# Performance work log

Hardware: AMD Instinct MI355X
Metric: run time of the kernel (lower is better)

Reference implementation:

```python
import jax, jax.numpy as jnp
import numpy as np

EPS = 1e-8  # torch CosineSimilarity default eps


def setup_inputs() -> dict:
    key = jax.random.key(0)
    k_emb, k_idx, k_w1, k_w2 = jax.random.split(key, 4)
    N, H, E = 50000, 128, 800000
    emb = jax.random.normal(k_emb, (N, H), dtype=jnp.float32)
    edge_index = jax.random.randint(k_idx, (2, E), 0, N, dtype=jnp.int64)
    # xavier_uniform for square H x H: limit = sqrt(6 / (H + H))
    lim = float(np.sqrt(6.0 / (H + H)))
    W1 = jax.random.uniform(k_w1, (H, H), dtype=jnp.float32, minval=-lim, maxval=lim)
    W2 = jax.random.uniform(k_w2, (H, H), dtype=jnp.float32, minval=-lim, maxval=lim)
    b1 = jnp.zeros((H,), dtype=jnp.float32)
    b2 = jnp.zeros((H,), dtype=jnp.float32)
    return {"emb": emb, "edge_index": edge_index, "W1": W1, "b1": b1, "W2": W2, "b2": b2}


def reference(emb, edge_index, W1, b1, W2, b2):
    col, row = edge_index[0], edge_index[1]

    def mlp(x):  # Linear -> (Dropout: identity at eval) -> ELU -> Linear
        h = jax.nn.elu(x @ W1.T + b1)
        return h @ W2.T + b2

    f1 = mlp(emb[col])  # [E, H]
    f2 = mlp(emb[row])  # [E, H]
    n1 = jnp.maximum(jnp.sqrt(jnp.sum(f1 * f1, axis=1)), EPS)
    n2 = jnp.maximum(jnp.sqrt(jnp.sum(f2 * f2, axis=1)), EPS)
    return jnp.sum(f1 * f2, axis=1) / (n1 * n2)  # [E]
```

## Files before the change

### kernel.cpp

```cpp
#include <hip/hip_runtime.h>
#include <math.h>

#define H 128
#define MROWS 64
#define XS 136

#if defined(__has_builtin)
# if __has_builtin(__builtin_amdgcn_sdot4)
#  define HAVE_SDOT4 1
# endif
#endif

typedef __attribute__((ext_vector_type(8))) short short8;
typedef __attribute__((ext_vector_type(4))) float floatx4;

__device__ __forceinline__ unsigned short f2bf(float f) {
    unsigned u = __float_as_uint(f);
    return (unsigned short)((u + 0x7FFFu + ((u >> 16) & 1u)) >> 16);
}

__global__ __launch_bounds__(256, 3) void mlp_mfma(
    const float* __restrict__ emb, const float* __restrict__ W1,
    const float* __restrict__ W2, const float* __restrict__ b1,
    const float* __restrict__ b2,
    signed char* __restrict__ qtab, float* __restrict__ scl, int N)
{
    __shared__ unsigned short Wl[H * XS];
    __shared__ unsigned short hs[MROWS * XS];

    const int tid   = threadIdx.x;
    const int wave  = tid >> 6, lane = tid & 63;
    const int quad  = lane >> 4, l15 = lane & 15;
    const int node0 = blockIdx.x * MROWS;

    const int  mrow = wave * 16 + l15;
    const int  grow = node0 + mrow;
    const bool rv   = grow < N;

    #pragma unroll
    for (int i = 0; i < 16; ++i) {
        int f = i * 1024 + tid * 4;
        int row = f >> 7, c = f & 127;
        float4 v = *(const float4*)(W1 + f);
        ushort4 b;
        b.x = f2bf(v.x); b.y = f2bf(v.y); b.z = f2bf(v.z); b.w = f2bf(v.w);
        *(ushort4*)(Wl + row * XS + c) = b;
    }

    short8 afr[4];
    #pragma unroll
    for (int ks = 0; ks < 4; ++ks) {
        float4 u0 = make_float4(0.f, 0.f, 0.f, 0.f);
        float4 u1 = make_float4(0.f, 0.f, 0.f, 0.f);
        if (rv) {
            const float* p = emb + (size_t)grow * H + ks * 32 + quad * 8;
            u0 = *(const float4*)p;
            u1 = *(const float4*)(p + 4);
        }
        short8 a;
        a[0] = (short)f2bf(u0.x); a[1] = (short)f2bf(u0.y);
        a[2] = (short)f2bf(u0.z); a[3] = (short)f2bf(u0.w);
        a[4] = (short)f2bf(u1.x); a[5] = (short)f2bf(u1.y);
        a[6] = (short)f2bf(u1.z); a[7] = (short)f2bf(u1.w);
        afr[ks] = a;
    }
    __syncthreads();

    #pragma unroll
    for (int nt = 0; nt < 8; ++nt) {
        floatx4 acc = {0.f, 0.f, 0.f, 0.f};
        #pragma unroll
        for (int ks = 0; ks < 4; ++ks) {
            short8 bfr = *(const short8*)(Wl + (nt * 16 + l15) * XS + ks * 32 + quad * 8);
            acc = __builtin_amdgcn_mfma_f32_16x16x32_bf16(afr[ks], bfr, acc, 0, 0, 0);
        }
        const int col = nt * 16 + l15;
        const float bb1 = b1[col];
        #pragma unroll
        for (int r = 0; r < 4; ++r) {
            float v = acc[r] + bb1;
            v = v > 0.f ? v : (__expf(v) - 1.f);
            hs[(wave * 16 + quad * 4 + r) * XS + col] = f2bf(v);
        }
    }
    __syncthreads();

    #pragma unroll
    for (int ks = 0; ks < 4; ++ks)
        afr[ks] = *(const short8*)(hs + mrow * XS + ks * 32 + quad * 8);
    #pragma unroll
    for (int i = 0; i < 16; ++i) {
        int f = i * 1024 + tid * 4;
        int row = f >> 7, c = f & 127;
        float4 v = *(const float4*)(W2 + f);
        ushort4 b;
        b.x = f2bf(v.x); b.y = f2bf(v.y); b.z = f2bf(v.z); b.w = f2bf(v.w);
        *(ushort4*)(Wl + row * XS + c) = b;
    }
    __syncthreads();

    floatx4 av[8];
    float sq[4] = {0.f, 0.f, 0.f, 0.f};
    float am[4] = {0.f, 0.f, 0.f, 0.f};
    #pragma unroll
    for (int nt = 0; nt < 8; ++nt) {
        floatx4 acc = {0.f, 0.f, 0.f, 0.f};
        #pragma unroll
        for (int ks = 0; ks < 4; ++ks) {
            short8 bfr = *(const short8*)(Wl + (nt * 16 + l15) * XS + ks * 32 + quad * 8);
            acc = __builtin_amdgcn_mfma_f32_16x16x32_bf16(afr[ks], bfr, acc, 0, 0, 0);
        }
        const float bb2 = b2[nt * 16 + l15];
        #pragma unroll
        for (int r = 0; r < 4; ++r) {
            float v = acc[r] + bb2;
            av[nt][r] = v;
            sq[r] += v * v;
            am[r] = fmaxf(am[r], fabsf(v));
        }
    }
    #pragma unroll
    for (int r = 0; r < 4; ++r) {
        float s = sq[r], a = am[r];
        #pragma unroll
        for (int m = 8; m; m >>= 1) {
            s += __shfl_xor(s, m);
            a = fmaxf(a, __shfl_xor(a, m));
        }
        sq[r] = s; am[r] = a;
    }
    #pragma unroll
    for (int r = 0; r < 4; ++r) {
        const int row = wave * 16 + quad * 4 + r;
        const int G = node0 + row;
        if (G < N) {
            const float a = fmaxf(am[r], 1e-20f);
            if (l15 == 0) {
                float nn = sqrtf(sq[r]);
                if (nn < 1e-8f) nn = 1e-8f;
                scl[G] = a / (nn * 127.f);
            }
            const float qs = 127.f / a;
            unsigned pk0 = 0, pk1 = 0;
            #pragma unroll
            for (int nt = 0; nt < 4; ++nt) {
                int q = (int)rintf(av[nt][r] * qs);
                q = q > 127 ? 127 : (q < -127 ? -127 : q);
                pk0 |= ((unsigned)(q & 255)) << (8 * nt);
            }
            #pragma unroll
            for (int nt = 4; nt < 8; ++nt) {
                int q = (int)rintf(av[nt][r] * qs);
                q = q > 127 ? 127 : (q < -127 ? -127 : q);
                pk1 |= ((unsigned)(q & 255)) << (8 * (nt - 4));
            }
            *(uint2*)(qtab + (size_t)G * H + l15 * 8) = make_uint2(pk0, pk1);
        }
    }
}

__device__ __forceinline__ int dot4s(unsigned a, unsigned b) {
    int s = 0;
    #pragma unroll
    for (int j = 0; j < 4; ++j)
        s += (int)((signed char)(a >> (8 * j))) * (int)((signed char)(b >> (8 * j)));
    return s;
}

__device__ __forceinline__ int dot16(uint4 a, uint4 b) {
#if defined(HAVE_SDOT4)
    int s = __builtin_amdgcn_sdot4((int)a.x, (int)b.x, 0, false);
    s = __builtin_amdgcn_sdot4((int)a.y, (int)b.y, s, false);
    s = __builtin_amdgcn_sdot4((int)a.z, (int)b.z, s, false);
    s = __builtin_amdgcn_sdot4((int)a.w, (int)b.w, s, false);
    return s;
#else
    return dot4s(a.x, b.x) + dot4s(a.y, b.y) + dot4s(a.z, b.z) + dot4s(a.w, b.w);
#endif
}

__global__ __launch_bounds__(256) void edge_cos(
    const int* __restrict__ ei, const signed char* __restrict__ qtab,
    const float* __restrict__ scl, float* __restrict__ out, int E)
{
    const int tid = threadIdx.x;
    const int sub = tid & 7;
    const int g   = (blockIdx.x * 256 + tid) >> 3;
    const int e0  = g * 4;
    if (e0 >= E) return;

    int cc[4], rr[4];
    #pragma unroll
    for (int k = 0; k < 4; ++k) {
        int e = e0 + k;
        if (e >= E) e = E - 1;
        cc[k] = __builtin_nontemporal_load(ei + e);
        rr[k] = __builtin_nontemporal_load(ei + e + E);
    }
    uint4 ua[4], ub[4];
    #pragma unroll
    for (int k = 0; k < 4; ++k) {
        ua[k] = *(const uint4*)(qtab + (size_t)cc[k] * H + sub * 16);
        ub[k] = *(const uint4*)(qtab + (size_t)rr[k] * H + sub * 16);
    }
    float sc[4];
    #pragma unroll
    for (int k = 0; k < 4; ++k) sc[k] = scl[cc[k]] * scl[rr[k]];

    #pragma unroll
    for (int k = 0; k < 4; ++k) {
        int s = dot16(ua[k], ub[k]);
        s += __shfl_xor(s, 4);
        s += __shfl_xor(s, 2);
        s += __shfl_xor(s, 1);
        if (sub == 0 && e0 + k < E)
            __builtin_nontemporal_store((float)s * sc[k], out + e0 + k);
    }
}

extern "C" void kernel_launch(void* const* d_in, const int* in_sizes, int n_in,
                              void* d_out, int out_size, void* d_ws, size_t ws_size,
                              hipStream_t stream) {
    const float* emb = (const float*)d_in[0];
    const int*   ei  = (const int*)d_in[1];
    const float* W1  = (const float*)d_in[2];
    const float* b1  = (const float*)d_in[3];
    const float* W2  = (const float*)d_in[4];
    const float* b2  = (const float*)d_in[5];
    float*       out = (float*)d_out;

    const int N = in_sizes[0] / H;
    const int E = in_sizes[1] / 2;

    signed char* qtab = (signed char*)d_ws;
    float*       sclp = (float*)(qtab + (size_t)N * H);

    mlp_mfma<<<(N + MROWS - 1) / MROWS, 256, 0, stream>>>(emb, W1, W2, b1, b2,
                                                          qtab, sclp, N);
    edge_cos<<<(E + 127) / 128, 256, 0, stream>>>(ei, qtab, sclp, out, E);
}
```

Before: 119.8 us.

## Pre-convert weights to bf16 once and use single-wave MLP blocks reading weights from global

```diff
diff --git a/kernel.cpp b/kernel.cpp
--- a/kernel.cpp
+++ b/kernel.cpp
@@ -2,7 +2,6 @@
 #include <math.h>
 
 #define H 128
-#define MROWS 64
 #define XS 136
 
 #if defined(__has_builtin)
@@ -13,39 +12,33 @@
 
 typedef __attribute__((ext_vector_type(8))) short short8;
 typedef __attribute__((ext_vector_type(4))) float floatx4;
+typedef __attribute__((ext_vector_type(4))) int intx4;
 
 __device__ __forceinline__ unsigned short f2bf(float f) {
     unsigned u = __float_as_uint(f);
     return (unsigned short)((u + 0x7FFFu + ((u >> 16) & 1u)) >> 16);
 }
 
-__global__ __launch_bounds__(256, 3) void mlp_mfma(
-    const float* __restrict__ emb, const float* __restrict__ W1,
-    const float* __restrict__ W2, const float* __restrict__ b1,
-    const float* __restrict__ b2,
+__global__ void prep_weights(const float* __restrict__ W1,
+                             const float* __restrict__ W2,
+                             unsigned short* __restrict__ Wbf) {
+    int i = blockIdx.x * 256 + threadIdx.x;
+    if (i < 16384)       Wbf[i] = f2bf(W1[i]);
+    else if (i < 32768)  Wbf[i] = f2bf(W2[i - 16384]);
+}
+
+__global__ __launch_bounds__(64, 4) void mlp_wave(
+    const float* __restrict__ emb, const unsigned short* __restrict__ Wbf,
+    const float* __restrict__ b1, const float* __restrict__ b2,
     signed char* __restrict__ qtab, float* __restrict__ scl, int N)
 {
-    __shared__ unsigned short Wl[H * XS];
-    __shared__ unsigned short hs[MROWS * XS];
-
-    const int tid   = threadIdx.x;
-    const int wave  = tid >> 6, lane = tid & 63;
+    __shared__ unsigned short hs[16 * XS];
+
+    const int lane  = threadIdx.x;
     const int quad  = lane >> 4, l15 = lane & 15;
-    const int node0 = blockIdx.x * MROWS;
-
-    const int  mrow = wave * 16 + l15;
-    const int  grow = node0 + mrow;
+    const int node0 = blockIdx.x * 16;
+    const int grow  = node0 + l15;
     const bool rv   = grow < N;
-
-    #pragma unroll
-    for (int i = 0; i < 16; ++i) {
-        int f = i * 1024 + tid * 4;
-        int row = f >> 7, c = f & 127;
-        float4 v = *(const float4*)(W1 + f);
-        ushort4 b;
-        b.x = f2bf(v.x); b.y = f2bf(v.y); b.z = f2bf(v.z); b.w = f2bf(v.w);
-        *(ushort4*)(Wl + row * XS + c) = b;
-    }
 
     short8 afr[4];
     #pragma unroll
@@ -64,14 +57,13 @@
         a[6] = (short)f2bf(u1.z); a[7] = (short)f2bf(u1.w);
         afr[ks] = a;
     }
-    __syncthreads();
 
     #pragma unroll
     for (int nt = 0; nt < 8; ++nt) {
         floatx4 acc = {0.f, 0.f, 0.f, 0.f};
         #pragma unroll
         for (int ks = 0; ks < 4; ++ks) {
-            short8 bfr = *(const short8*)(Wl + (nt * 16 + l15) * XS + ks * 32 + quad * 8);
+            short8 bfr = *(const short8*)(Wbf + (nt * 16 + l15) * H + ks * 32 + quad * 8);
             acc = __builtin_amdgcn_mfma_f32_16x16x32_bf16(afr[ks], bfr, acc, 0, 0, 0);
         }
         const int col = nt * 16 + l15;
@@ -80,24 +72,14 @@
         for (int r = 0; r < 4; ++r) {
             float v = acc[r] + bb1;
             v = v > 0.f ? v : (__expf(v) - 1.f);
-            hs[(wave * 16 + quad * 4 + r) * XS + col] = f2bf(v);
+            hs[(quad * 4 + r) * XS + col] = f2bf(v);
         }
     }
     __syncthreads();
 
     #pragma unroll
     for (int ks = 0; ks < 4; ++ks)
-        afr[ks] = *(const short8*)(hs + mrow * XS + ks * 32 + quad * 8);
-    #pragma unroll
-    for (int i = 0; i < 16; ++i) {
-        int f = i * 1024 + tid * 4;
-        int row = f >> 7, c = f & 127;
-        float4 v = *(const float4*)(W2 + f);
-        ushort4 b;
-        b.x = f2bf(v.x); b.y = f2bf(v.y); b.z = f2bf(v.z); b.w = f2bf(v.w);
-        *(ushort4*)(Wl + row * XS + c) = b;
-    }
-    __syncthreads();
+        afr[ks] = *(const short8*)(hs + l15 * XS + ks * 32 + quad * 8);
 
     floatx4 av[8];
     float sq[4] = {0.f, 0.f, 0.f, 0.f};
@@ -107,7 +89,7 @@
         floatx4 acc = {0.f, 0.f, 0.f, 0.f};
         #pragma unroll
         for (int ks = 0; ks < 4; ++ks) {
-            short8 bfr = *(const short8*)(Wl + (nt * 16 + l15) * XS + ks * 32 + quad * 8);
+            short8 bfr = *(const short8*)(Wbf + 16384 + (nt * 16 + l15) * H + ks * 32 + quad * 8);
             acc = __builtin_amdgcn_mfma_f32_16x16x32_bf16(afr[ks], bfr, acc, 0, 0, 0);
         }
         const float bb2 = b2[nt * 16 + l15];
@@ -131,7 +113,7 @@
     }
     #pragma unroll
     for (int r = 0; r < 4; ++r) {
-        const int row = wave * 16 + quad * 4 + r;
+        const int row = quad * 4 + r;
         const int G = node0 + row;
         if (G < N) {
             const float a = fmaxf(am[r], 1e-20f);
@@ -190,12 +172,18 @@
     if (e0 >= E) return;
 
     int cc[4], rr[4];
-    #pragma unroll
-    for (int k = 0; k < 4; ++k) {
-        int e = e0 + k;
-        if (e >= E) e = E - 1;
-        cc[k] = __builtin_nontemporal_load(ei + e);
-        rr[k] = __builtin_nontemporal_load(ei + e + E);
+    if (e0 + 3 < E) {
+        intx4 c4 = __builtin_nontemporal_load((const intx4*)(ei + e0));
+        intx4 r4 = __builtin_nontemporal_load((const intx4*)(ei + E + e0));
+        cc[0] = c4.x; cc[1] = c4.y; cc[2] = c4.z; cc[3] = c4.w;
+        rr[0] = r4.x; rr[1] = r4.y; rr[2] = r4.z; rr[3] = r4.w;
+    } else {
+        #pragma unroll
+        for (int k = 0; k < 4; ++k) {
+            int e = e0 + k; if (e >= E) e = E - 1;
+            cc[k] = __builtin_nontemporal_load(ei + e);
+            rr[k] = __builtin_nontemporal_load(ei + e + E);
+        }
     }
     uint4 ua[4], ub[4];
     #pragma unroll
@@ -232,10 +220,11 @@
     const int N = in_sizes[0] / H;
     const int E = in_sizes[1] / 2;
 
-    signed char* qtab = (signed char*)d_ws;
-    float*       sclp = (float*)(qtab + (size_t)N * H);
-
-    mlp_mfma<<<(N + MROWS - 1) / MROWS, 256, 0, stream>>>(emb, W1, W2, b1, b2,
-                                                          qtab, sclp, N);
+    unsigned short* Wbf  = (unsigned short*)d_ws;
+    signed char*    qtab = (signed char*)(Wbf + 32768);
+    float*          sclp = (float*)(qtab + (size_t)N * H);
+
+    prep_weights<<<128, 256, 0, stream>>>(W1, W2, Wbf);
+    mlp_wave<<<(N + 15) / 16, 64, 0, stream>>>(emb, Wbf, b1, b2, qtab, sclp, N);
     edge_cos<<<(E + 127) / 128, 256, 0, stream>>>(ei, qtab, sclp, out, E);
 }
```

After: 133.3 us. 1.11x slower.

## Split quantized node table into two halves and run edge dot in two passes

Applied to the files above, without the earlier changes.

```diff
diff --git a/kernel.cpp b/kernel.cpp
--- a/kernel.cpp
+++ b/kernel.cpp
@@ -13,6 +13,7 @@
 
 typedef __attribute__((ext_vector_type(8))) short short8;
 typedef __attribute__((ext_vector_type(4))) float floatx4;
+typedef __attribute__((ext_vector_type(4))) int intx4;
 
 __device__ __forceinline__ unsigned short f2bf(float f) {
     unsigned u = __float_as_uint(f);
@@ -23,7 +24,8 @@
     const float* __restrict__ emb, const float* __restrict__ W1,
     const float* __restrict__ W2, const float* __restrict__ b1,
     const float* __restrict__ b2,
-    signed char* __restrict__ qtab, float* __restrict__ scl, int N)
+    signed char* __restrict__ qtabA, signed char* __restrict__ qtabB,
+    float* __restrict__ scl, int N)
 {
     __shared__ unsigned short Wl[H * XS];
     __shared__ unsigned short hs[MROWS * XS];
@@ -129,6 +131,7 @@
         }
         sq[r] = s; am[r] = a;
     }
+    signed char* half = (l15 < 8) ? qtabA : qtabB;
     #pragma unroll
     for (int r = 0; r < 4; ++r) {
         const int row = wave * 16 + quad * 4 + r;
@@ -154,7 +157,7 @@
                 q = q > 127 ? 127 : (q < -127 ? -127 : q);
                 pk1 |= ((unsigned)(q & 255)) << (8 * (nt - 4));
             }
-            *(uint2*)(qtab + (size_t)G * H + l15 * 8) = make_uint2(pk0, pk1);
+            *(uint2*)(half + (size_t)G * 64 + (l15 & 7) * 8) = make_uint2(pk0, pk1);
         }
     }
 }
@@ -179,42 +182,108 @@
 #endif
 }
 
-__global__ __launch_bounds__(256) void edge_cos(
-    const int* __restrict__ ei, const signed char* __restrict__ qtab,
-    const float* __restrict__ scl, float* __restrict__ out, int E)
+__device__ __forceinline__ void load_idx4(const int* __restrict__ ei, int E,
+                                          int e0, int cc[4], int rr[4]) {
+    if (e0 + 3 < E) {
+        intx4 c4 = __builtin_nontemporal_load((const intx4*)(ei + e0));
+        intx4 r4 = __builtin_nontemporal_load((const intx4*)(ei + E + e0));
+        cc[0] = c4.x; cc[1] = c4.y; cc[2] = c4.z; cc[3] = c4.w;
+        rr[0] = r4.x; rr[1] = r4.y; rr[2] = r4.z; rr[3] = r4.w;
+    } else {
+        #pragma unroll
+        for (int k = 0; k < 4; ++k) {
+            int e = e0 + k; if (e >= E) e = E - 1;
+            cc[k] = __builtin_nontemporal_load(ei + e);
+            rr[k] = __builtin_nontemporal_load(ei + e + E);
+        }
+    }
+}
+
+__global__ __launch_bounds__(256) void edge_dotA(
+    const int* __restrict__ ei, const signed char* __restrict__ qtabA,
+    int* __restrict__ part, int E)
 {
     const int tid = threadIdx.x;
-    const int sub = tid & 7;
-    const int g   = (blockIdx.x * 256 + tid) >> 3;
+    const int sub = tid & 3;
+    const int g   = (blockIdx.x * 256 + tid) >> 2;
     const int e0  = g * 4;
     if (e0 >= E) return;
 
     int cc[4], rr[4];
+    load_idx4(ei, E, e0, cc, rr);
+
+    uint4 ua[4], ub[4];
     #pragma unroll
     for (int k = 0; k < 4; ++k) {
-        int e = e0 + k;
-        if (e >= E) e = E - 1;
-        cc[k] = __builtin_nontemporal_load(ei + e);
-        rr[k] = __builtin_nontemporal_load(ei + e + E);
-    }
+        ua[k] = *(const uint4*)(qtabA + (size_t)cc[k] * 64 + sub * 16);
+        ub[k] = *(const uint4*)(qtabA + (size_t)rr[k] * 64 + sub * 16);
+    }
+    int s[4];
+    #pragma unroll
+    for (int k = 0; k < 4; ++k) {
+        int v = dot16(ua[k], ub[k]);
+        v += __shfl_xor(v, 2);
+        v += __shfl_xor(v, 1);
+        s[k] = v;
+    }
+    if (sub == 0) {
+        if (e0 + 3 < E) {
+            intx4 p; p.x = s[0]; p.y = s[1]; p.z = s[2]; p.w = s[3];
+            __builtin_nontemporal_store(p, (intx4*)(part + e0));
+        } else {
+            #pragma unroll
+            for (int k = 0; k < 4; ++k)
+                if (e0 + k < E) __builtin_nontemporal_store(s[k], part + e0 + k);
+        }
+    }
+}
+
+__global__ __launch_bounds__(256) void edge_dotB(
+    const int* __restrict__ ei, const signed char* __restrict__ qtabB,
+    const float* __restrict__ scl, const int* __restrict__ part,
+    float* __restrict__ out, int E)
+{
+    const int tid = threadIdx.x;
+    const int sub = tid & 3;
+    const int g   = (blockIdx.x * 256 + tid) >> 2;
+    const int e0  = g * 4;
+    if (e0 >= E) return;
+
+    int cc[4], rr[4];
+    load_idx4(ei, E, e0, cc, rr);
+
     uint4 ua[4], ub[4];
     #pragma unroll
     for (int k = 0; k < 4; ++k) {
-        ua[k] = *(const uint4*)(qtab + (size_t)cc[k] * H + sub * 16);
-        ub[k] = *(const uint4*)(qtab + (size_t)rr[k] * H + sub * 16);
-    }
-    float sc[4];
-    #pragma unroll
-    for (int k = 0; k < 4; ++k) sc[k] = scl[cc[k]] * scl[rr[k]];
-
+        ua[k] = *(const uint4*)(qtabB + (size_t)cc[k] * 64 + sub * 16);
+        ub[k] = *(const uint4*)(qtabB + (size_t)rr[k] * 64 + sub * 16);
+    }
+    int s[4];
     #pragma unroll
     for (int k = 0; k < 4; ++k) {
-        int s = dot16(ua[k], ub[k]);
-        s += __shfl_xor(s, 4);
-        s += __shfl_xor(s, 2);
-        s += __shfl_xor(s, 1);
-        if (sub == 0 && e0 + k < E)
-            __builtin_nontemporal_store((float)s * sc[k], out + e0 + k);
+        int v = dot16(ua[k], ub[k]);
+        v += __shfl_xor(v, 2);
+        v += __shfl_xor(v, 1);
+        s[k] = v;
+    }
+    if (sub == 0) {
+        if (e0 + 3 < E) {
+            intx4 p = __builtin_nontemporal_load((const intx4*)(part + e0));
+            floatx4 o;
+            o.x = (float)(s[0] + p.x) * scl[cc[0]] * scl[rr[0]];
+            o.y = (float)(s[1] + p.y) * scl[cc[1]] * scl[rr[1]];
+            o.z = (float)(s[2] + p.z) * scl[cc[2]] * scl[rr[2]];
+            o.w = (float)(s[3] + p.w) * scl[cc[3]] * scl[rr[3]];
+            __builtin_nontemporal_store(o, (floatx4*)(out + e0));
+        } else {
+            #pragma unroll
+            for (int k = 0; k < 4; ++k)
+                if (e0 + k < E) {
+                    int pv = __builtin_nontemporal_load(part + e0 + k);
+                    float vv = (float)(s[k] + pv) * scl[cc[k]] * scl[rr[k]];
+                    __builtin_nontemporal_store(vv, out + e0 + k);
+                }
+        }
     }
 }
 
@@ -232,10 +301,13 @@
     const int N = in_sizes[0] / H;
     const int E = in_sizes[1] / 2;
 
-    signed char* qtab = (signed char*)d_ws;
-    float*       sclp = (float*)(qtab + (size_t)N * H);
+    signed char* qtabA = (signed char*)d_ws;
+    signed char* qtabB = qtabA + (size_t)N * 64;
+    float*       sclp  = (float*)(qtabB + (size_t)N * 64);
+    int*         part  = (int*)(sclp + N);
 
     mlp_mfma<<<(N + MROWS - 1) / MROWS, 256, 0, stream>>>(emb, W1, W2, b1, b2,
-                                                          qtab, sclp, N);
-    edge_cos<<<(E + 127) / 128, 256, 0, stream>>>(ei, qtab, sclp, out, E);
-}
+                                                          qtabA, qtabB, sclp, N);
+    edge_dotA<<<(E + 255) / 256, 256, 0, stream>>>(ei, qtabA, part, E);
+    edge_dotB<<<(E + 255) / 256, 256, 0, stream>>>(ei, qtabB, sclp, part, out, E);
+}
```

After: 125.5 us. 4.7% more time.
